# Optimization experiments

Hardware: AMD Instinct MI355X
Metric: run time of the kernel (lower is better)

Reference implementation:

```python
import jax, jax.numpy as jnp
import numpy as np
from jax import lax

B, E, K, CAP, NC, TC = 512, 8, 2, 160, 10, 256
EPS = 1e-5
CHANS = [(32, 3), (64, 32), (128, 64), (256, 128)]

def _conv(x, w, b):
    y = lax.conv_general_dilated(x, w, (1, 1), 'SAME', dimension_numbers=('NCHW', 'OIHW', 'NCHW'))
    return y + b[None, :, None, None]

def _bn(x, g, bt, m, v):
    # eval-mode batchnorm with running stats
    s = g / jnp.sqrt(v + EPS)
    return x * s[None, :, None, None] + (bt - m * s)[None, :, None, None]

def _maxpool2(x):
    return lax.reduce_window(x, -jnp.inf, lax.max, (1, 1, 2, 2), (1, 1, 2, 2), 'VALID')

def _trunk(x, ps):
    for i in range(4):
        w, b, g, bt, rm, rv = ps[i]
        x = jax.nn.relu(_bn(_conv(x, w, b), g, bt, rm, rv))
        if i in (1, 3):
            x = _maxpool2(x)
    return x.mean(axis=(2, 3))  # AdaptiveAvgPool2d(1) + Flatten -> [B, TC]

def _route(conf):
    total_needed = B * K
    per_cycle = (total_needed + 3) // 4

    def item_body(c, idx):
        D, ec, sc, assigned, cyc = c
        b, j = idx // E, idx % E
        ok = (~D[b, j]) & (ec[j] < CAP) & (sc[b] < K) & (cyc < per_cycle) & (assigned < total_needed)
        oki = ok.astype(jnp.int32)
        return (D.at[b, j].set(D[b, j] | ok), ec.at[j].add(oki), sc.at[b].add(oki), assigned + oki, cyc + oki), None

    def cycle_body(carry, _):
        D, ec, sc, assigned, current = carry
        order = jnp.argsort(-current.reshape(-1)).astype(jnp.int32)  # descending sort of B*E scores
        (D, ec, sc, assigned, _), _ = lax.scan(item_body, (D, ec, sc, assigned, jnp.int32(0)), order)
        current = conf * (1.0 - ec.astype(jnp.float32) / CAP)[None, :]
        return (D, ec, sc, assigned, current), None

    init = (jnp.zeros((B, E), bool), jnp.zeros((E,), jnp.int32), jnp.zeros((B,), jnp.int32), jnp.int32(0), conf)
    (D, ec, sc, assigned, cur), _ = lax.scan(cycle_body, init, None, length=4)
    return D

def _forward(x, params, cls_w, cls_b):
    feats = _trunk(x, params)                                     # [B, TC]
    logits = jnp.einsum('bd,ecd->bec', feats, cls_w) + cls_b[None]  # [B, E, NC]
    logp = jax.nn.log_softmax(logits, axis=2)
    conf = (jnp.exp(logp) * logp).sum(axis=2)                     # -entropy  [B, E]
    D = _route(lax.stop_gradient(conf))                           # [B, E] bool
    w = jnp.where(D, conf, 0.0)
    final = jnp.einsum('be,bec->bc', w, logits)
    norm = jnp.maximum(D.sum(axis=1, keepdims=True).astype(jnp.float32), 1.0)
    return final / norm, conf, D

def setup_inputs():
    key = jax.random.key(0)
    ks = jax.random.split(key, 8)
    inp = {'x': jax.random.normal(ks[0], (B, 3, 32, 32), jnp.float32)}
    for i, (co, ci) in enumerate(CHANS):
        inp[f'w{i}'] = jax.random.normal(ks[1 + i], (co, ci, 3, 3), jnp.float32) * (2.0 / (ci * 9)) ** 0.5
        inp[f'b{i}'] = jnp.zeros((co,), jnp.float32)
        inp[f'g{i}'] = jnp.ones((co,), jnp.float32)
        inp[f'bt{i}'] = jnp.zeros((co,), jnp.float32)
        inp[f'rm{i}'] = jnp.zeros((co,), jnp.float32)
        inp[f'rv{i}'] = jnp.ones((co,), jnp.float32)
    inp['cls_w'] = jax.random.normal(ks[5], (E, NC, TC), jnp.float32) / TC ** 0.5
    inp['cls_b'] = jnp.zeros((E, NC), jnp.float32)
    return inp

def reference(x, w0, b0, g0, bt0, rm0, rv0, w1, b1, g1, bt1, rm1, rv1, w2, b2, g2, bt2, rm2, rv2, w3, b3, g3, bt3, rm3, rv3, cls_w, cls_b):
    params = [(w0, b0, g0, bt0, rm0, rv0), (w1, b1, g1, bt1, rm1, rv1), (w2, b2, g2, bt2, rm2, rv2), (w3, b3, g3, bt3, rm3, rv3)]
    return _forward(x, params, cls_w, cls_b)
```

## Files before the change

### kernel.cpp

```cpp
#include <hip/hip_runtime.h>
#include <hip/hip_bf16.h>
#include <cstdint>
#include <cstddef>

#define EPSV 1e-5f
typedef unsigned short u16;
using short8 = __attribute__((ext_vector_type(8))) short;
using f32x4  = __attribute__((ext_vector_type(4))) float;

typedef __attribute__((address_space(1))) void* gp1;
typedef __attribute__((address_space(3))) void* lp3;

__device__ __forceinline__ void gload16(const void* g, void* l) {
    __builtin_amdgcn_global_load_lds((gp1)(void*)g, (lp3)l, 16, 0, 0);
}
__device__ __forceinline__ u16 f2bf(float v) {
    __hip_bfloat16 h = __float2bfloat16(v);
    return *reinterpret_cast<u16*>(&h);
}
__device__ __forceinline__ float bf2f(u16 u) {
    __hip_bfloat16 h; *reinterpret_cast<u16*>(&h) = u;
    return __bfloat162float(h);
}

template<int PH2, int PW2, int C>
__global__ __launch_bounds__(256) void ring_kernel(u16* __restrict__ bh, u16* __restrict__ bl)
{
    constexpr int RN = 2 * PW2 + 2 * (PH2 - 2);
    constexpr int C8 = C / 8;
    int id = blockIdx.x * 256 + (int)threadIdx.x;
    if (id >= 512 * RN * C8) return;
    int c8 = id % C8; int t = id / C8;
    int rp = t % RN;  int im = t / RN;
    int py, px;
    if (rp < PW2)            { py = 0;       px = rp; }
    else if (rp < 2 * PW2)   { py = PH2 - 1; px = rp - PW2; }
    else { int rr = rp - 2 * PW2; py = 1 + (rr >> 1); px = (rr & 1) ? (PW2 - 1) : 0; }
    size_t off = ((size_t)(im * PH2 + py) * PW2 + px) * C + c8 * 8;
    uint4 z = {0u, 0u, 0u, 0u};
    *(uint4*)(bh + off) = z;
    *(uint4*)(bl + off) = z;
}

template<int CIN, int COUT>
__global__ __launch_bounds__(256) void wprep_kernel(
    const float* __restrict__ w, const float* __restrict__ b,
    const float* __restrict__ g, const float* __restrict__ bt,
    const float* __restrict__ rm, const float* __restrict__ rv,
    u16* __restrict__ WH, u16* __restrict__ WL, float* __restrict__ bias)
{
    int id = blockIdx.x * 256 + (int)threadIdx.x;
    if (id >= CIN * COUT) return;
    int co = id / CIN, ci = id % CIN;
    float s = g[co] / sqrtf(rv[co] + EPSV);
    #pragma unroll
    for (int k = 0; k < 9; ++k) {
        float v = w[((size_t)co * CIN + ci) * 9 + k] * s;
        u16 hh = f2bf(v);
        size_t o = ((size_t)k * COUT + co) * CIN + ci;
        WH[o] = hh;
        WL[o] = f2bf(v - bf2f(hh));
    }
    if (ci == 0) bias[co] = (b[co] - rm[co]) * s + bt[co];
}

__global__ __launch_bounds__(256) void conv0_kernel(
    const float* __restrict__ x, const float* __restrict__ w,
    const float* __restrict__ bias, const float* __restrict__ g,
    const float* __restrict__ bt, const float* __restrict__ rm,
    const float* __restrict__ rv, u16* __restrict__ Oh, u16* __restrict__ Ol)
{
    const int blk = blockIdx.x;
    const int img = blk >> 2;
    const int p = ((blk & 3) << 8) | (int)threadIdx.x;
    const int y = p >> 5, xx = p & 31;
    const float* xin = x + (size_t)img * 3 * 1024;
    float xv[3][9];
    #pragma unroll
    for (int ci = 0; ci < 3; ++ci)
      #pragma unroll
      for (int ky = 0; ky < 3; ++ky)
        #pragma unroll
        for (int kx = 0; kx < 3; ++kx) {
            int yy = y + ky - 1, xc = xx + kx - 1;
            bool v = (yy >= 0) && (yy < 32) && (xc >= 0) && (xc < 32);
            xv[ci][ky * 3 + kx] = v ? xin[ci * 1024 + yy * 32 + xc] : 0.0f;
        }
    union { u16 u[32]; uint4 v4[4]; } oh, ol;
    #pragma unroll
    for (int co = 0; co < 32; ++co) {
        float s = g[co] / sqrtf(rv[co] + EPSV);
        float c = (bias[co] - rm[co]) * s + bt[co];
        float acc = 0.f;
        #pragma unroll
        for (int ci = 0; ci < 3; ++ci)
          #pragma unroll
          for (int k = 0; k < 9; ++k)
            acc += w[(co * 3 + ci) * 9 + k] * xv[ci][k];
        float v = acc * s + c;
        v = v > 0.f ? v : 0.f;
        u16 hh = f2bf(v);
        oh.u[co] = hh;
        ol.u[co] = f2bf(v - bf2f(hh));
    }
    size_t po = ((size_t)(img * 34 + y + 1) * 34 + xx + 1) * 32;
    #pragma unroll
    for (int q = 0; q < 4; ++q) {
        ((uint4*)(Oh + po))[q] = oh.v4[q];
        ((uint4*)(Ol + po))[q] = ol.v4[q];
    }
}

template<int CIN, int COUT, int H, int W, int BM, int BN, int MODE>
__global__ __launch_bounds__(256, 2) void convM_kernel(
    const u16* __restrict__ Ah, const u16* __restrict__ Al,
    const u16* __restrict__ Wh, const u16* __restrict__ Wl,
    const float* __restrict__ bias,
    u16* __restrict__ Oh, u16* __restrict__ Ol, float* __restrict__ featsPart)
{
    constexpr int KC = CIN / 32;
    constexpr int ROWS = BM / W;
    constexpr int WM = BM / 64;
    constexpr int WN = 4 / WM;
    constexpr int NT = BN / (WN * 16);
    constexpr int PW = W + 2;
    constexpr int AT = (ROWS + 2) * PW;
    constexpr int ACH = AT * 4;
    constexpr int BCH = BN * 4;
    constexpr int LW2 = (W == 32) ? 5 : 4;
    constexpr int MPI = (H * W) / BM;

    __shared__ u16 lA[2][AT * 32];
    __shared__ u16 lB[2][BN * 32];

    const int tid = (int)threadIdx.x;
    const int lane = tid & 63;
    const int wv = tid >> 6;
    const int wm = (WM == 4) ? wv : (wv >> 1);
    const int wn = (WM == 4) ? 0 : (wv & 1);
    const int l15 = lane & 15, quad = lane >> 4;

    const int mblk = (int)blockIdx.x, nblk = (int)blockIdx.y;
    const int img = mblk / MPI;
    const int y0 = (mblk % MPI) * ROWS;
    const size_t imgRow = (size_t)img * (H + 2);

    f32x4 acc[4][NT];
    f32x4 zz = {0.f, 0.f, 0.f, 0.f};
    #pragma unroll
    for (int i = 0; i < 4; ++i)
      #pragma unroll
      for (int j = 0; j < NT; ++j) acc[i][j] = zz;

    for (int cb = 0; cb < KC; ++cb) {
        __syncthreads();
        #pragma unroll
        for (int it = 0; it < (ACH + 255) / 256; ++it) {
            int id = it * 256 + tid;
            if (id < ACH) {
                int p = id >> 2;
                int s = ((id & 3) - (p >> 1)) & 3;
                int yy = p / PW, xx = p - yy * PW;
                size_t ge = ((imgRow + y0 + yy) * PW + xx) * CIN + cb * 32 + s * 8;
                u16* ld = (u16*)&lA[0][0] + (size_t)(it * 256 + wv * 64) * 8;
                gload16(Ah + ge, ld);
                gload16(Al + ge, ld + AT * 32);
            }
        }
        for (int sh = 0; sh < 9; ++sh) {
            const int ky = sh / 3, kx = sh - 3 * (sh / 3);
            if (sh) __syncthreads();
            #pragma unroll
            for (int it = 0; it < (BCH + 255) / 256; ++it) {
                int id = it * 256 + tid;
                if (id < BCH) {
                    int n = id >> 2;
                    int s = ((id & 3) - (n >> 1)) & 3;
                    size_t ge = ((size_t)sh * COUT + nblk * BN + n) * CIN + cb * 32 + s * 8;
                    u16* ld = (u16*)&lB[0][0] + (size_t)(it * 256 + wv * 64) * 8;
                    gload16(Wh + ge, ld);
                    gload16(Wl + ge, ld + BN * 32);
                }
            }
            __syncthreads();
            short8 bh[NT], bl[NT];
            #pragma unroll
            for (int nt = 0; nt < NT; ++nt) {
                int nrow = wn * (NT * 16) + nt * 16 + l15;
                int boff = nrow * 32 + (((quad + (nrow >> 1)) & 3) * 8);
                bh[nt] = *(const short8*)&lB[0][boff];
                bl[nt] = *(const short8*)&lB[1][boff];
            }
            #pragma unroll
            for (int mt = 0; mt < 4; ++mt) {
                int p = wm * 64 + mt * 16 + l15;
                int yl = p >> LW2, xl = p & (W - 1);
                int pix = (yl + ky) * PW + xl + kx;
                int aoff = pix * 32 + (((quad + (pix >> 1)) & 3) * 8);
                short8 ah = *(const short8*)&lA[0][aoff];
                short8 al = *(const short8*)&lA[1][aoff];
                #pragma unroll
                for (int nt = 0; nt < NT; ++nt) {
                    acc[mt][nt] = __builtin_amdgcn_mfma_f32_16x16x32_bf16(ah, bh[nt], acc[mt][nt], 0, 0, 0);
                    acc[mt][nt] = __builtin_amdgcn_mfma_f32_16x16x32_bf16(ah, bl[nt], acc[mt][nt], 0, 0, 0);
                    acc[mt][nt] = __builtin_amdgcn_mfma_f32_16x16x32_bf16(al, bh[nt], acc[mt][nt], 0, 0, 0);
                }
            }
        }
    }

    if constexpr (MODE == 0) {
        #pragma unroll
        for (int mt = 0; mt < 4; ++mt) {
            int pbase = wm * 64 + mt * 16 + quad * 4;
            int yy = pbase >> LW2;
            #pragma unroll
            for (int nt = 0; nt < NT; ++nt) {
                int n = nblk * BN + wn * (NT * 16) + nt * 16 + l15;
                float bs = bias[n];
                #pragma unroll
                for (int r = 0; r < 4; ++r) {
                    int xx = (pbase & (W - 1)) + r;
                    float v = acc[mt][nt][r] + bs; v = v > 0.f ? v : 0.f;
                    size_t oo = ((size_t)(img * (H + 2) + y0 + yy + 1) * (W + 2) + xx + 1) * COUT + n;
                    u16 hh = f2bf(v);
                    Oh[oo] = hh;
                    Ol[oo] = f2bf(v - bf2f(hh));
                }
            }
        }
    } else if constexpr (MODE == 1) {
        #pragma unroll
        for (int nt = 0; nt < NT; ++nt) {
            int n = nt * 16 + l15;
            float bs = bias[n];
            #pragma unroll
            for (int mb = 0; mb < 2; ++mb) {
                #pragma unroll
                for (int xp = 0; xp < 2; ++xp) {
                    float v = fmaxf(fmaxf(acc[mb][nt][2 * xp], acc[mb][nt][2 * xp + 1]),
                                    fmaxf(acc[mb + 2][nt][2 * xp], acc[mb + 2][nt][2 * xp + 1]));
                    v += bs; v = v > 0.f ? v : 0.f;
                    int py = (y0 >> 1) + wm;
                    int px = mb * 8 + quad * 2 + xp;
                    size_t oo = ((size_t)(img * 18 + py + 1) * 18 + px + 1) * COUT + n;
                    u16 hh = f2bf(v);
                    Oh[oo] = hh;
                    Ol[oo] = f2bf(v - bf2f(hh));
                }
            }
        }
    } else {
        __shared__ float fbuf[2][BN];
        #pragma unroll
        for (int nt = 0; nt < NT; ++nt) {
            int col = wn * (NT * 16) + nt * 16 + l15;
            float bs = bias[nblk * BN + col];
            float s = 0.f;
            #pragma unroll
            for (int mp = 0; mp < 2; ++mp)
              #pragma unroll
              for (int xp = 0; xp < 2; ++xp) {
                  float v = fmaxf(fmaxf(acc[2 * mp][nt][2 * xp], acc[2 * mp][nt][2 * xp + 1]),
                                  fmaxf(acc[2 * mp + 1][nt][2 * xp], acc[2 * mp + 1][nt][2 * xp + 1]));
                  v += bs; v = v > 0.f ? v : 0.f;
                  s += v;
              }
            s += __shfl_xor(s, 16, 64);
            s += __shfl_xor(s, 32, 64);
            if (quad == 0) fbuf[wm][col] = s;
        }
        __syncthreads();
        if (tid < BN) {
            float f = (fbuf[0][tid] + fbuf[1][tid]) * (1.0f / 64.0f);
            featsPart[((size_t)(mblk % MPI) * 512 + img) * 256 + nblk * BN + tid] = f;
        }
    }
}

__global__ __launch_bounds__(128) void head_kernel(
    const float* __restrict__ featsPart, const float* __restrict__ cls_w,
    const float* __restrict__ cls_b, float* __restrict__ logits,
    float* __restrict__ conf)
{
    __shared__ float f[256];
    __shared__ float wt[80 * 65];
    __shared__ float lg[80];
    const int b = blockIdx.x, tid = (int)threadIdx.x;
    f[tid]       = featsPart[b * 256 + tid]       + featsPart[131072 + b * 256 + tid];
    f[tid + 128] = featsPart[b * 256 + tid + 128] + featsPart[131072 + b * 256 + tid + 128];
    float acc = 0.f;
    for (int ch = 0; ch < 4; ++ch) {
        __syncthreads();
        for (int q = tid; q < 80 * 64; q += 128) {
            int r = q >> 6, cc = q & 63;
            wt[r * 65 + cc] = cls_w[r * 256 + ch * 64 + cc];
        }
        __syncthreads();
        if (tid < 80) {
            #pragma unroll 8
            for (int dd = 0; dd < 64; ++dd)
                acc += wt[tid * 65 + dd] * f[ch * 64 + dd];
        }
    }
    if (tid < 80) {
        acc += cls_b[tid];
        logits[b * 80 + tid] = acc;
        lg[tid] = acc;
    }
    __syncthreads();
    if (tid < 80 && (tid % 10) == 0) {
        const int e = tid / 10;
        float m = lg[e * 10];
        for (int cc = 1; cc < 10; ++cc) m = fmaxf(m, lg[e * 10 + cc]);
        float ssum = 0.f;
        for (int cc = 0; cc < 10; ++cc) ssum += expf(lg[e * 10 + cc] - m);
        float lz = m + logf(ssum);
        float cf = 0.f;
        for (int cc = 0; cc < 10; ++cc) {
            float lp = lg[e * 10 + cc] - lz;
            cf += expf(lp) * lp;
        }
        conf[b * 8 + e] = cf;
    }
}

__global__ __launch_bounds__(256) void presort_kernel(
    const float* __restrict__ confG, u16* __restrict__ sidx0)
{
    __shared__ float v[512];
    __shared__ u16 bi[512];
    const int j = (int)blockIdx.x, tid = (int)threadIdx.x;
    for (int r = tid; r < 512; r += 256) { v[r] = confG[r * 8 + j]; bi[r] = (u16)r; }
    for (int k = 2; k <= 512; k <<= 1)
        for (int jj = k >> 1; jj > 0; jj >>= 1) {
            __syncthreads();
            int i = ((tid & ~(jj - 1)) << 1) | (tid & (jj - 1));
            int p = i | jj;
            float va = v[i], vb = v[p];
            u16 ia = bi[i], ib = bi[p];
            bool first = (va > vb) || (va == vb && ia < ib);
            bool up = (i & k) == 0;
            if (up ? !first : first) { v[i] = vb; v[p] = va; bi[i] = ib; bi[p] = ia; }
        }
    __syncthreads();
    for (int r = tid; r < 512; r += 256)
        sidx0[j * 512 + r] = (u16)(bi[r] * 8 + j);
}

__global__ __launch_bounds__(1024) void route_kernel(
    const float* __restrict__ confG,
    const float* __restrict__ logitsG,
    const u16*   __restrict__ sidx0,
    float* __restrict__ outv)
{
    __shared__ float valById[4096];
    __shared__ float sv[4096];
    __shared__ u16 P[4096];
    __shared__ u16 mA[4096];
    __shared__ u16 mB[4096];
    __shared__ unsigned char Dls[512];
    __shared__ int ec[8];
    __shared__ int assignedS;
    const int tid = (int)threadIdx.x;

    for (int t = tid; t < 4096; t += 1024) {
        valById[t] = confG[t];
        P[t] = sidx0[t];
    }
    if (tid < 512) Dls[tid] = 0;
    if (tid < 8) ec[tid] = 0;
    if (tid == 0) assignedS = 0;

    auto earlier = [&](u16 a, u16 b) -> bool {
        float va = sv[a], vb = sv[b];
        return (va > vb) || (va == vb && a < b);
    };
    auto mergeChunk = [&](const u16* X, const u16* Y, int n, int o0, u16* out) {
        int lo = o0 - n; if (lo < 0) lo = 0;
        int hi = o0 < n ? o0 : n;
        while (lo < hi) {
            int mid = (lo + hi) >> 1;
            if (earlier(X[mid], Y[o0 - 1 - mid])) lo = mid + 1; else hi = mid;
        }
        int i = lo, jj = o0 - lo;
        #pragma unroll
        for (int q = 0; q < 4; ++q) {
            u16 xc = X[i < n ? i : (n - 1)];
            u16 yc = Y[jj < n ? jj : (n - 1)];
            bool takeX = (jj >= n) || ((i < n) && earlier(xc, yc));
            out[q] = takeX ? xc : yc;
            if (takeX) ++i; else ++jj;
        }
    };

    for (int cycle = 0; cycle < 4; ++cycle) {
        __syncthreads();
        for (int t = tid; t < 4096; t += 1024) {
            float sc = 1.0f - ((float)ec[t & 7]) / 160.0f;
            sv[t] = valById[t] * sc;
        }
        __syncthreads();
        {
            int g = tid << 2;
            int p = g >> 10, o0 = g & 1023;
            mergeChunk(&P[(p << 1) * 512], &P[(p << 1) * 512 + 512], 512, o0, &mA[(p << 10) + o0]);
        }
        __syncthreads();
        {
            int g = tid << 2;
            int p = g >> 11, o0 = g & 2047;
            mergeChunk(&mA[p << 11], &mA[(p << 11) + 1024], 1024, o0, &mB[(p << 11) + o0]);
        }
        __syncthreads();
        {
            int o0 = tid << 2;
            mergeChunk(&mB[0], &mB[2048], 2048, o0, &mA[o0]);
        }
        __syncthreads();
        if (tid < 64) {
            const int lane = tid;
            int cyc = 0;
            int assigned = assignedS;
            for (int chunk = 0; chunk < 64; ++chunk) {
                if (cyc >= 256 || assigned >= 1024) break;
                int id = mA[(chunk << 6) | lane];
                int b = id >> 3, j = id & 7;
                unsigned d = Dls[b];
                bool notA = ((d >> j) & 1) == 0;
                int ecj = ec[j];
                int scb = __popc(d & 255);
                unsigned long long sb = ~0ull;
                #pragma unroll
                for (int t2 = 0; t2 < 9; ++t2) {
                    unsigned long long bl = __ballot((b >> t2) & 1);
                    sb &= ((b >> t2) & 1) ? bl : ~bl;
                }
                unsigned long long jb0 = __ballot(j & 1);
                unsigned long long jb1 = __ballot((j >> 1) & 1);
                unsigned long long jb2 = __ballot((j >> 2) & 1);
                unsigned long long sj = ((j & 1) ? jb0 : ~jb0) &
                                        ((j & 2) ? jb1 : ~jb1) &
                                        ((j & 4) ? jb2 : ~jb2);
                unsigned long long earlierM = (1ull << lane) - 1ull;
                bool ok = notA && (ecj < 160) && (scb < 2);
                unsigned long long okm = __ballot(ok);
                for (int it = 0; it < 64; ++it) {
                    unsigned long long em = okm & earlierM;
                    int aE = __popcll(em & sj);
                    int aS = __popcll(em & sb);
                    int aC = __popcll(em);
                    bool ok2 = notA && (ecj + aE) < 160 && (scb + aS) < 2 &&
                               (cyc + aC) < 256 && (assigned + aC) < 1024;
                    unsigned long long okm2 = __ballot(ok2);
                    ok = ok2;
                    if (okm2 == okm) break;
                    okm = okm2;
                }
                int add = __popcll(okm);
                if (lane < 8) {
                    unsigned long long mj = ((lane & 1) ? jb0 : ~jb0) &
                                            ((lane & 2) ? jb1 : ~jb1) &
                                            ((lane & 4) ? jb2 : ~jb2);
                    int c2 = __popcll(mj & okm);
                    if (c2) ec[lane] += c2;
                }
                if (ok) {
                    unsigned long long grp = okm & sb;
                    if (lane == __builtin_ctzll(grp)) {
                        unsigned orb = 0;
                        #pragma unroll
                        for (int jj2 = 0; jj2 < 8; ++jj2) {
                            unsigned long long mj2 = ((jj2 & 1) ? jb0 : ~jb0) &
                                                     ((jj2 & 2) ? jb1 : ~jb1) &
                                                     ((jj2 & 4) ? jb2 : ~jb2);
                            if (mj2 & grp) orb |= (1u << jj2);
                        }
                        Dls[b] = (unsigned char)(d | orb);
                    }
                }
                cyc += add;
                assigned += add;
                __threadfence_block();
            }
            if (lane == 0) assignedS = assigned;
        }
    }
    __syncthreads();

    for (int o = tid; o < 5120; o += 1024) {
        int b = o / 10, c = o - b * 10;
        unsigned d = Dls[b];
        float norm = fmaxf((float)__popc(d & 255), 1.0f);
        float sum = 0.f;
        #pragma unroll
        for (int e = 0; e < 8; ++e)
            if ((d >> e) & 1)
                sum += confG[b * 8 + e] * logitsG[(b * 8 + e) * 10 + c];
        outv[o] = sum / norm;
    }
    for (int t = tid; t < 4096; t += 1024) {
        outv[5120 + t] = confG[t];
        outv[9216 + t] = (float)((Dls[t >> 3] >> (t & 7)) & 1);
    }
}

extern "C" void kernel_launch(void* const* d_in, const int* in_sizes, int n_in,
                              void* d_out, int out_size, void* d_ws, size_t ws_size,
                              hipStream_t stream)
{
    const float* x    = (const float*)d_in[0];
    const float* w0   = (const float*)d_in[1];
    const float* b0   = (const float*)d_in[2];
    const float* g0   = (const float*)d_in[3];
    const float* bt0  = (const float*)d_in[4];
    const float* rm0  = (const float*)d_in[5];
    const float* rv0  = (const float*)d_in[6];
    const float* w1   = (const float*)d_in[7];
    const float* b1   = (const float*)d_in[8];
    const float* g1   = (const float*)d_in[9];
    const float* bt1  = (const float*)d_in[10];
    const float* rm1  = (const float*)d_in[11];
    const float* rv1  = (const float*)d_in[12];
    const float* w2   = (const float*)d_in[13];
    const float* b2   = (const float*)d_in[14];
    const float* g2   = (const float*)d_in[15];
    const float* bt2  = (const float*)d_in[16];
    const float* rm2  = (const float*)d_in[17];
    const float* rv2  = (const float*)d_in[18];
    const float* w3   = (const float*)d_in[19];
    const float* b3   = (const float*)d_in[20];
    const float* g3   = (const float*)d_in[21];
    const float* bt3  = (const float*)d_in[22];
    const float* rm3  = (const float*)d_in[23];
    const float* rv3  = (const float*)d_in[24];
    const float* cls_w = (const float*)d_in[25];
    const float* cls_b = (const float*)d_in[26];
    float* outp = (float*)d_out;

    char* ws = (char*)d_ws;
    u16* A1H = (u16*)(ws);
    u16* A1L = (u16*)(ws + 21233664);
    u16* A0H = (u16*)(ws + 42467328);
    u16* A0L = (u16*)(ws + 42467328 + 37879808);
    u16* A2H = (u16*)(ws + 42467328);
    u16* A2L = (u16*)(ws + 42467328 + 42467328);
    u16* W1H = (u16*)(ws + 127401984);
    u16* W1L = (u16*)(ws + 127438848);
    u16* W2H = (u16*)(ws + 127475712);
    u16* W2L = (u16*)(ws + 127623168);
    u16* W3H = (u16*)(ws + 127770624);
    u16* W3L = (u16*)(ws + 128360448);
    float* BS1 = (float*)(ws + 128950272);
    float* BS2 = (float*)(ws + 128950528);
    float* BS3 = (float*)(ws + 128951040);
    float* featsPart = (float*)(ws + 128952064);
    float* logits    = (float*)(ws + 130000640);
    float* conf      = (float*)(ws + 130164480);
    u16* sidx0 = (u16*)(ws + 42467328);

    ring_kernel<34, 34, 32><<<(512 * 132 * 4 + 255) / 256, 256, 0, stream>>>(A0H, A0L);
    ring_kernel<18, 18, 64><<<(512 * 68 * 8 + 255) / 256, 256, 0, stream>>>(A1H, A1L);
    wprep_kernel<32, 64><<<8, 256, 0, stream>>>(w1, b1, g1, bt1, rm1, rv1, W1H, W1L, BS1);
    wprep_kernel<64, 128><<<32, 256, 0, stream>>>(w2, b2, g2, bt2, rm2, rv2, W2H, W2L, BS2);
    wprep_kernel<128, 256><<<128, 256, 0, stream>>>(w3, b3, g3, bt3, rm3, rv3, W3H, W3L, BS3);

    conv0_kernel<<<2048, 256, 0, stream>>>(x, w0, b0, g0, bt0, rm0, rv0, A0H, A0L);
    convM_kernel<32, 64, 32, 32, 256, 64, 1>
        <<<dim3(2048, 1), 256, 0, stream>>>(A0H, A0L, W1H, W1L, BS1, A1H, A1L, nullptr);
    ring_kernel<18, 18, 128><<<(512 * 68 * 16 + 255) / 256, 256, 0, stream>>>(A2H, A2L);
    convM_kernel<64, 128, 16, 16, 128, 64, 0>
        <<<dim3(1024, 2), 256, 0, stream>>>(A1H, A1L, W2H, W2L, BS2, A2H, A2L, nullptr);
    convM_kernel<128, 256, 16, 16, 128, 64, 2>
        <<<dim3(1024, 4), 256, 0, stream>>>(A2H, A2L, W3H, W3L, BS3, nullptr, nullptr, featsPart);
    head_kernel<<<512, 128, 0, stream>>>(featsPart, cls_w, cls_b, logits, conf);
    presort_kernel<<<8, 256, 0, stream>>>(conf, sidx0);
    route_kernel<<<1, 1024, 0, stream>>>(conf, logits, sidx0, outp);
}
```

Before: 623.3 us.

## Stage three kx weight taps per barrier and widen conv2 N tile

The conv kernel now loads the weights for all three kx taps of a kernel row into LDS at once. This cuts the barrier/load phases per channel block from nine to three and lets three taps of MFMA work run between syncs. Separately, the second conv layer switches from BN=64 to BN=128 with half the grid in N, so each block reuses its staged activation tile across twice as many output channels. The cost is triple the B-tile LDS footprint, which may lower occupancy under launch_bounds(256,2), and fewer blocks for conv2.

```diff
diff --git a/kernel.cpp b/kernel.cpp
--- a/kernel.cpp
+++ b/kernel.cpp
@@ -126,12 +126,12 @@
     constexpr int PW = W + 2;
     constexpr int AT = (ROWS + 2) * PW;
     constexpr int ACH = AT * 4;
-    constexpr int BCH = BN * 4;
+    constexpr int BCH3 = 3 * BN * 4;
     constexpr int LW2 = (W == 32) ? 5 : 4;
     constexpr int MPI = (H * W) / BM;
 
     __shared__ u16 lA[2][AT * 32];
-    __shared__ u16 lB[2][BN * 32];
+    __shared__ u16 lB[2][3 * BN * 32];
 
     const int tid = (int)threadIdx.x;
     const int lane = tid & 63;
@@ -152,8 +152,7 @@
       #pragma unroll
       for (int j = 0; j < NT; ++j) acc[i][j] = zz;
 
-    for (int cb = 0; cb < KC; ++cb) {
-        __syncthreads();
+    auto stageA = [&](int cb) {
         #pragma unroll
         for (int it = 0; it < (ACH + 255) / 256; ++it) {
             int id = it * 256 + tid;
@@ -167,43 +166,60 @@
                 gload16(Al + ge, ld + AT * 32);
             }
         }
-        for (int sh = 0; sh < 9; ++sh) {
-            const int ky = sh / 3, kx = sh - 3 * (sh / 3);
-            if (sh) __syncthreads();
+    };
+    auto stageB3 = [&](int cb, int ky) {
+        #pragma unroll
+        for (int it = 0; it < (BCH3 + 255) / 256; ++it) {
+            int id = it * 256 + tid;
+            if (id < BCH3) {
+                int kx = id / (BN * 4);
+                int r = id - kx * (BN * 4);
+                int n = r >> 2;
+                int s = ((r & 3) - (n >> 1)) & 3;
+                size_t ge = ((size_t)(ky * 3 + kx) * COUT + nblk * BN + n) * CIN + cb * 32 + s * 8;
+                u16* ld = (u16*)&lB[0][0] + (size_t)(it * 256 + wv * 64) * 8;
+                gload16(Wh + ge, ld);
+                gload16(Wl + ge, ld + 3 * BN * 32);
+            }
+        }
+    };
+
+    for (int cb = 0; cb < KC; ++cb) {
+        __syncthreads();
+        stageA(cb);
+        stageB3(cb, 0);
+        __syncthreads();
+        #pragma unroll
+        for (int ky = 0; ky < 3; ++ky) {
+            if (ky) {
+                __syncthreads();
+                stageB3(cb, ky);
+                __syncthreads();
+            }
             #pragma unroll
-            for (int it = 0; it < (BCH + 255) / 256; ++it) {
-                int id = it * 256 + tid;
-                if (id < BCH) {
-                    int n = id >> 2;
-                    int s = ((id & 3) - (n >> 1)) & 3;
-                    size_t ge = ((size_t)sh * COUT + nblk * BN + n) * CIN + cb * 32 + s * 8;
-                    u16* ld = (u16*)&lB[0][0] + (size_t)(it * 256 + wv * 64) * 8;
-                    gload16(Wh + ge, ld);
-                    gload16(Wl + ge, ld + BN * 32);
-                }
-            }
-            __syncthreads();
-            short8 bh[NT], bl[NT];
-            #pragma unroll
-            for (int nt = 0; nt < NT; ++nt) {
-                int nrow = wn * (NT * 16) + nt * 16 + l15;
-                int boff = nrow * 32 + (((quad + (nrow >> 1)) & 3) * 8);
-                bh[nt] = *(const short8*)&lB[0][boff];
-                bl[nt] = *(const short8*)&lB[1][boff];
-            }
-            #pragma unroll
-            for (int mt = 0; mt < 4; ++mt) {
-                int p = wm * 64 + mt * 16 + l15;
-                int yl = p >> LW2, xl = p & (W - 1);
-                int pix = (yl + ky) * PW + xl + kx;
-                int aoff = pix * 32 + (((quad + (pix >> 1)) & 3) * 8);
-                short8 ah = *(const short8*)&lA[0][aoff];
-                short8 al = *(const short8*)&lA[1][aoff];
+            for (int kx = 0; kx < 3; ++kx) {
+                short8 bh[NT], bl[NT];
                 #pragma unroll
                 for (int nt = 0; nt < NT; ++nt) {
-                    acc[mt][nt] = __builtin_amdgcn_mfma_f32_16x16x32_bf16(ah, bh[nt], acc[mt][nt], 0, 0, 0);
-                    acc[mt][nt] = __builtin_amdgcn_mfma_f32_16x16x32_bf16(ah, bl[nt], acc[mt][nt], 0, 0, 0);
-                    acc[mt][nt] = __builtin_amdgcn_mfma_f32_16x16x32_bf16(al, bh[nt], acc[mt][nt], 0, 0, 0);
+                    int nrow = wn * (NT * 16) + nt * 16 + l15;
+                    int boff = kx * BN * 32 + nrow * 32 + (((quad + (nrow >> 1)) & 3) * 8);
+                    bh[nt] = *(const short8*)&lB[0][boff];
+                    bl[nt] = *(const short8*)&lB[1][boff];
+                }
+                #pragma unroll
+                for (int mt = 0; mt < 4; ++mt) {
+                    int p = wm * 64 + mt * 16 + l15;
+                    int yl = p >> LW2, xl = p & (W - 1);
+                    int pix = (yl + ky) * PW + xl + kx;
+                    int aoff = pix * 32 + (((quad + (pix >> 1)) & 3) * 8);
+                    short8 ah = *(const short8*)&lA[0][aoff];
+                    short8 al = *(const short8*)&lA[1][aoff];
+                    #pragma unroll
+                    for (int nt = 0; nt < NT; ++nt) {
+                        acc[mt][nt] = __builtin_amdgcn_mfma_f32_16x16x32_bf16(ah, bh[nt], acc[mt][nt], 0, 0, 0);
+                        acc[mt][nt] = __builtin_amdgcn_mfma_f32_16x16x32_bf16(ah, bl[nt], acc[mt][nt], 0, 0, 0);
+                        acc[mt][nt] = __builtin_amdgcn_mfma_f32_16x16x32_bf16(al, bh[nt], acc[mt][nt], 0, 0, 0);
+                    }
                 }
             }
         }
@@ -569,8 +585,8 @@
     convM_kernel<32, 64, 32, 32, 256, 64, 1>
         <<<dim3(2048, 1), 256, 0, stream>>>(A0H, A0L, W1H, W1L, BS1, A1H, A1L, nullptr);
     ring_kernel<18, 18, 128><<<(512 * 68 * 16 + 255) / 256, 256, 0, stream>>>(A2H, A2L);
-    convM_kernel<64, 128, 16, 16, 128, 64, 0>
-        <<<dim3(1024, 2), 256, 0, stream>>>(A1H, A1L, W2H, W2L, BS2, A2H, A2L, nullptr);
+    convM_kernel<64, 128, 16, 16, 128, 128, 0>
+        <<<dim3(1024, 1), 256, 0, stream>>>(A1H, A1L, W2H, W2L, BS2, A2H, A2L, nullptr);
     convM_kernel<128, 256, 16, 16, 128, 64, 2>
         <<<dim3(1024, 4), 256, 0, stream>>>(A2H, A2L, W3H, W3L, BS3, nullptr, nullptr, featsPart);
     head_kernel<<<512, 128, 0, stream>>>(featsPart, cls_w, cls_b, logits, conf);
```

New measurement: 610.9 us. -2.0%, faster.
